# Performance work log

Measured on AMD Instinct MI355X. Metric: run time of the kernel, lower is better.

The kernel has to match this reference:

```python
import jax, jax.numpy as jnp
import numpy as np

NEG_SLOPE = 0.2


def setup_inputs() -> dict:
    key = jax.random.key(0)
    ks = jax.random.split(key, 6)
    N, E, IN, OUT = 100000, 1600000, 128, 64
    x = jax.random.normal(ks[0], (N, IN), dtype=jnp.float32)
    edge_index = jax.random.randint(ks[1], (2, E), 0, N, dtype=jnp.int64)
    W = jax.random.normal(ks[2], (IN, OUT), dtype=jnp.float32) * (1.0 / np.sqrt(IN))
    att_src = jax.random.normal(ks[3], (OUT,), dtype=jnp.float32) * (1.0 / np.sqrt(OUT))
    att_dst = jax.random.normal(ks[4], (OUT,), dtype=jnp.float32) * (1.0 / np.sqrt(OUT))
    bias = jnp.zeros((OUT,), dtype=jnp.float32)
    return {"x": x, "edge_index": edge_index, "W": W,
            "att_src": att_src, "att_dst": att_dst, "bias": bias}


def reference(x, edge_index, W, att_src, att_dst, bias):
    N = x.shape[0]
    # PyG GATConv default: add self loops
    loop = jnp.arange(N, dtype=edge_index.dtype)
    src = jnp.concatenate([edge_index[0], loop])  # message sources j
    dst = jnp.concatenate([edge_index[1], loop])  # message targets i

    h = x @ W                                      # [N, out]
    a_s = h @ att_src                              # [N]
    a_d = h @ att_dst                              # [N]

    # per-edge unnormalized attention logits (leaky relu, slope 0.2)
    e = jax.nn.leaky_relu(a_s[src] + a_d[dst], negative_slope=NEG_SLOPE)  # [E+N]

    # segment softmax over edges grouped by destination node
    seg_max = jax.ops.segment_max(e, dst, num_segments=N)  # [N]
    e_exp = jnp.exp(e - seg_max[dst])
    seg_sum = jax.ops.segment_sum(e_exp, dst, num_segments=N)  # [N], >0 via self loops
    alpha = e_exp / seg_sum[dst]                                # [E+N]

    # weighted scatter-add aggregation
    out = jax.ops.segment_sum(alpha[:, None] * h[src], dst, num_segments=N)  # [N, out]
    return out + bias
```

## Files before the change

### kernel.cpp

```cpp
#include <hip/hip_runtime.h>
#include <hip/hip_bf16.h>
#include <math.h>

#define NEG_SLOPE 0.2f
#define BSH    7
#define BNODES 128
#define CAP    2560
#define MAXB   1024
#define NCHUNK 256
#define CEMAX  6272
#define SMEMB  39424

typedef __attribute__((ext_vector_type(8))) short bf16x8;
typedef __attribute__((ext_vector_type(4))) float f32x4;

__device__ __forceinline__ float leaky(float v) { return v >= 0.0f ? v : NEG_SLOPE * v; }
__device__ __forceinline__ int clampi(int v, int lo, int hi) {
    return v < lo ? lo : (v > hi ? hi : v);
}
__device__ __forceinline__ float bflo(unsigned u) { return __uint_as_float(u << 16); }
__device__ __forceinline__ float bfhi(unsigned u) { return __uint_as_float(u & 0xFFFF0000u); }
__device__ __forceinline__ unsigned short f2bf(float f) {
    unsigned u = __float_as_uint(f);
    return (unsigned short)((u + 0x7FFFu + ((u >> 16) & 1u)) >> 16);
}
__device__ __forceinline__ bf16x8 pack8(float4 a, float4 b) {
    bf16x8 r;
    r[0] = (short)f2bf(a.x); r[1] = (short)f2bf(a.y);
    r[2] = (short)f2bf(a.z); r[3] = (short)f2bf(a.w);
    r[4] = (short)f2bf(b.x); r[5] = (short)f2bf(b.y);
    r[6] = (short)f2bf(b.z); r[7] = (short)f2bf(b.w);
    return r;
}

__global__ __launch_bounds__(512) void k_fused(
    const float* __restrict__ x, const float* __restrict__ W,
    const float* __restrict__ att_src, const float* __restrict__ att_dst,
    __hip_bfloat16* __restrict__ h, float* __restrict__ a_s,
    float* __restrict__ a_d, const int* __restrict__ ei,
    unsigned* __restrict__ binned, int* __restrict__ offc,
    int N, int E, int CE, int nb_lin)
{
    __shared__ int4 smem4[SMEMB / 16];
    const int tid = threadIdx.x;

    if ((int)blockIdx.x < nb_lin) {
        short* wlds = (short*)smem4;

        for (int idx = tid; idx < 1024; idx += 512) {
            int f = idx >> 6, L = idx & 63;
            int t = f >> 2, k0i = f & 3;
            int kbase = k0i * 32 + (L >> 4) * 8;
            int c = t * 16 + (L & 15);
            unsigned short v[8];
#pragma unroll
            for (int j = 0; j < 8; ++j) v[j] = f2bf(W[(kbase + j) * 64 + c]);
            uint4 p;
            p.x = (unsigned)v[0] | ((unsigned)v[1] << 16);
            p.y = (unsigned)v[2] | ((unsigned)v[3] << 16);
            p.z = (unsigned)v[4] | ((unsigned)v[5] << 16);
            p.w = (unsigned)v[6] | ((unsigned)v[7] << 16);
            ((uint4*)wlds)[idx] = p;
        }
        __syncthreads();

        const int lane = tid & 63;
        const int w    = tid >> 6;
        const int base = blockIdx.x * 128 + w * 16;
        const int m    = lane & 15;
        const int quad = lane >> 4;

        int rowc = min(base + m, N - 1);
        const float4* xr = (const float4*)x + (size_t)rowc * 32;

        bf16x8 afrag[4];
#pragma unroll
        for (int k0i = 0; k0i < 4; ++k0i) {
            float4 f0 = xr[k0i * 8 + quad * 2 + 0];
            float4 f1 = xr[k0i * 8 + quad * 2 + 1];
            afrag[k0i] = pack8(f0, f1);
        }

        f32x4 acc[4];
#pragma unroll
        for (int t = 0; t < 4; ++t) acc[t] = (f32x4){0.f, 0.f, 0.f, 0.f};

        const bf16x8* wf = (const bf16x8*)wlds;
#pragma unroll
        for (int t = 0; t < 4; ++t) {
#pragma unroll
            for (int k0i = 0; k0i < 4; ++k0i) {
                bf16x8 bfr = wf[(t * 4 + k0i) * 64 + lane];
                acc[t] = __builtin_amdgcn_mfma_f32_16x16x32_bf16(afrag[k0i], bfr, acc[t], 0, 0, 0);
            }
        }

        float ps[4] = {0.f, 0.f, 0.f, 0.f};
        float pd[4] = {0.f, 0.f, 0.f, 0.f};
#pragma unroll
        for (int t = 0; t < 4; ++t) {
            float as_c = att_src[t * 16 + m];
            float ad_c = att_dst[t * 16 + m];
#pragma unroll
            for (int q = 0; q < 4; ++q) {
                ps[q] = fmaf(acc[t][q], as_c, ps[q]);
                pd[q] = fmaf(acc[t][q], ad_c, pd[q]);
            }
        }
#pragma unroll
        for (int t = 0; t < 4; ++t) {
#pragma unroll
            for (int q = 0; q < 4; ++q) {
                int n = base + quad * 4 + q;
                if (n < N) h[(size_t)n * 64 + t * 16 + m] = __float2bfloat16(acc[t][q]);
            }
        }
#pragma unroll
        for (int q = 0; q < 4; ++q) {
            ps[q] += __shfl_xor(ps[q], 1, 64);
            ps[q] += __shfl_xor(ps[q], 2, 64);
            ps[q] += __shfl_xor(ps[q], 4, 64);
            ps[q] += __shfl_xor(ps[q], 8, 64);
            pd[q] += __shfl_xor(pd[q], 1, 64);
            pd[q] += __shfl_xor(pd[q], 2, 64);
            pd[q] += __shfl_xor(pd[q], 4, 64);
            pd[q] += __shfl_xor(pd[q], 8, 64);
        }
        if (m == 0) {
#pragma unroll
            for (int q = 0; q < 4; ++q) {
                int n = base + quad * 4 + q;
                if (n < N) { a_s[n] = ps[q]; a_d[n] = pd[q]; }
            }
        }
    } else {
        int* hist = (int*)smem4;
        int* off  = hist + MAXB;
        int* cur  = off + MAXB;
        int* s    = cur + MAXB;
        unsigned* stage = (unsigned*)(s + 512);

        const int c  = (int)blockIdx.x - nb_lin;
        const int e0 = c * CE;
        const int e1 = min(E, e0 + CE);
        const int ne = e1 - e0;

        for (int i = tid; i < MAXB; i += 512) hist[i] = 0;
        __syncthreads();
        for (int e = e0 + tid; e < e1; e += 512) {
            int dst = clampi(ei[E + e], 0, N - 1);
            atomicAdd(&hist[dst >> BSH], 1);
        }
        __syncthreads();
        int a0 = hist[2 * tid], a1 = hist[2 * tid + 1];
        int psum = a0 + a1;
        s[tid] = psum;
        __syncthreads();
        for (int d = 1; d < 512; d <<= 1) {
            int v = (tid >= d) ? s[tid - d] : 0;
            __syncthreads();
            s[tid] += v;
            __syncthreads();
        }
        int excl = s[tid] - psum;
        off[2 * tid]     = excl;
        off[2 * tid + 1] = excl + a0;
        cur[2 * tid]     = excl;
        cur[2 * tid + 1] = excl + a0;
        __syncthreads();
        for (int e = e0 + tid; e < e1; e += 512) {
            int src = clampi(ei[e],     0, N - 1);
            int dst = clampi(ei[E + e], 0, N - 1);
            int pos = atomicAdd(&cur[dst >> BSH], 1);
            stage[clampi(pos, 0, CEMAX - 1)] =
                ((unsigned)(dst & (BNODES - 1)) << 17) | (unsigned)src;
        }
        __syncthreads();
        for (int i = tid; i < ne; i += 512) binned[e0 + i] = stage[i];
        int* oc = offc + (size_t)c * (MAXB + 1);
        for (int i = tid; i < MAXB; i += 512) oc[i] = off[i];
        if (tid == 0) oc[MAXB] = ne;
    }
}

__global__ __launch_bounds__(512) void k_agg(
    const unsigned* __restrict__ binned, const int* __restrict__ offc,
    const float* __restrict__ a_s, const float* __restrict__ a_d,
    const __hip_bfloat16* __restrict__ hm, const float* __restrict__ bias,
    float* __restrict__ out, int N, int CE)
{
    __shared__ int   cnt[BNODES];
    __shared__ int   st[BNODES];
    __shared__ int   cur[BNODES];
    __shared__ float lsum[BNODES];
    __shared__ float wsl[BNODES];
    __shared__ float adl[BNODES];
    __shared__ int   runScan[NCHUNK + 1];
    __shared__ int   gbase[NCHUNK];
    __shared__ int   sc[NCHUNK];
    __shared__ unsigned eraw[CAP];
    __shared__ uint2 ew[CAP];

    const int tid   = threadIdx.x;
    const int b     = blockIdx.x;
    const int nbase = b << BSH;

    if (tid < BNODES) {
        cnt[tid] = 0;
        int n = nbase + tid;
        float as = 0.f, ad = 0.f;
        if (n < N) { as = a_s[n]; ad = a_d[n]; }
        adl[tid] = ad;
        float v = (n < N) ? __expf(leaky(as + ad)) : 0.f;
        wsl[tid]  = v;
        lsum[tid] = v;
    }
    int rc = 0;
    if (tid < NCHUNK) {
        const int* oc = offc + (size_t)tid * (MAXB + 1);
        int o0 = clampi(oc[b],     0, CE);
        int o1 = clampi(oc[b + 1], o0, CE);
        rc = o1 - o0;
        gbase[tid] = tid * CE + o0;
        sc[tid] = rc;
    }
    __syncthreads();
    for (int d = 1; d < NCHUNK; d <<= 1) {
        int v = (tid < NCHUNK && tid >= d) ? sc[tid - d] : 0;
        __syncthreads();
        if (tid < NCHUNK) sc[tid] += v;
        __syncthreads();
    }
    if (tid < NCHUNK) runScan[tid] = sc[tid] - rc;
    if (tid == NCHUNK - 1) runScan[NCHUNK] = sc[NCHUNK - 1];
    __syncthreads();
    int n_e = runScan[NCHUNK];
    if (n_e > CAP) n_e = CAP;

    for (int i = tid; i < n_e; i += 512) {
        int c = 0;
#pragma unroll
        for (int stp = NCHUNK >> 1; stp >= 1; stp >>= 1)
            if (runScan[c + stp] <= i) c += stp;
        eraw[i] = binned[(size_t)gbase[c] + (i - runScan[c])];
    }
    __syncthreads();
    for (int i = tid; i < n_e; i += 512)
        atomicAdd(&cnt[(eraw[i] >> 17) & (BNODES - 1)], 1);
    __syncthreads();
    if (tid < BNODES) st[tid] = cnt[tid];
    __syncthreads();
    for (int d = 1; d < BNODES; d <<= 1) {
        int v = (tid < BNODES && tid >= d) ? st[tid - d] : 0;
        __syncthreads();
        if (tid < BNODES) st[tid] += v;
        __syncthreads();
    }
    if (tid < BNODES) { st[tid] -= cnt[tid]; cur[tid] = st[tid]; }
    __syncthreads();
    for (int i = tid; i < n_e; i += 512) {
        unsigned pk = eraw[i];
        int ld  = (int)(pk >> 17) & (BNODES - 1);
        int src = (int)(pk & 0x1FFFFu);
        float wv = __expf(leaky(a_s[src] + adl[ld]));
        int pos = atomicAdd(&cur[ld], 1);
        if (pos < CAP) ew[pos] = make_uint2((unsigned)src, __float_as_uint(wv));
        atomicAdd(&lsum[ld], wv);
    }
    __syncthreads();

    const int lane = tid & 63;
    const int w    = tid >> 6;
    const int q    = lane & 7;
    const int p    = lane >> 3;
    const uint4*  h4 = (const uint4*)hm;
    const float4* b4 = (const float4*)bias;
    const float4 bb0 = b4[2 * q];
    const float4 bb1 = b4[2 * q + 1];

#pragma unroll 1
    for (int t = 0; t < 2; ++t) {
        int ln = t * 64 + w * 8 + p;
        int n  = nbase + ln;
        if (n >= N) continue;
        int deg = cnt[ln];
        int s0  = st[ln];
        if (s0 > CAP) s0 = CAP;
        if (deg > CAP - s0) deg = CAP - s0;

        float wself = wsl[ln];
        uint4 U = h4[(size_t)n * 8 + q];
        float acc0 = wself * bflo(U.x), acc1 = wself * bfhi(U.x);
        float acc2 = wself * bflo(U.y), acc3 = wself * bfhi(U.y);
        float acc4 = wself * bflo(U.z), acc5 = wself * bfhi(U.z);
        float acc6 = wself * bflo(U.w), acc7 = wself * bfhi(U.w);

        float wc = 0.f;
        if (deg > 0) {
            uint2 e0 = ew[s0];
            wc = __uint_as_float(e0.y);
            U  = h4[(size_t)e0.x * 8 + q];
        }
        for (int j = 0; j < deg; ++j) {
            uint4 U2 = make_uint4(0u, 0u, 0u, 0u);
            float w2 = 0.f;
            if (j + 1 < deg) {
                uint2 e1 = ew[s0 + j + 1];
                w2 = __uint_as_float(e1.y);
                U2 = h4[(size_t)e1.x * 8 + q];
            }
            acc0 = fmaf(wc, bflo(U.x), acc0);
            acc1 = fmaf(wc, bfhi(U.x), acc1);
            acc2 = fmaf(wc, bflo(U.y), acc2);
            acc3 = fmaf(wc, bfhi(U.y), acc3);
            acc4 = fmaf(wc, bflo(U.z), acc4);
            acc5 = fmaf(wc, bfhi(U.z), acc5);
            acc6 = fmaf(wc, bflo(U.w), acc6);
            acc7 = fmaf(wc, bfhi(U.w), acc7);
            U = U2; wc = w2;
        }

        float inv = 1.0f / lsum[ln];
        float4 o0, o1;
        o0.x = bb0.x + acc0 * inv;
        o0.y = bb0.y + acc1 * inv;
        o0.z = bb0.z + acc2 * inv;
        o0.w = bb0.w + acc3 * inv;
        o1.x = bb1.x + acc4 * inv;
        o1.y = bb1.y + acc5 * inv;
        o1.z = bb1.z + acc6 * inv;
        o1.w = bb1.w + acc7 * inv;
        float4* o4 = (float4*)out;
        o4[(size_t)n * 16 + 2 * q + 0] = o0;
        o4[(size_t)n * 16 + 2 * q + 1] = o1;
    }
}

extern "C" void kernel_launch(void* const* d_in, const int* in_sizes, int n_in,
                              void* d_out, int out_size, void* d_ws, size_t ws_size,
                              hipStream_t stream)
{
    const float* x       = (const float*)d_in[0];
    const int*   ei      = (const int*)d_in[1];
    const float* W       = (const float*)d_in[2];
    const float* att_src = (const float*)d_in[3];
    const float* att_dst = (const float*)d_in[4];
    const float* bias    = (const float*)d_in[5];
    float*       out     = (float*)d_out;

    const int N = in_sizes[0] / 128;
    const int E = in_sizes[1] / 2;

    __hip_bfloat16* h      = (__hip_bfloat16*)d_ws;
    float*          a_s    = (float*)(h + (size_t)N * 64);
    float*          a_d    = a_s + N;
    int*            offc   = (int*)(a_d + N);
    unsigned*       binned = (unsigned*)(offc + NCHUNK * (MAXB + 1));

    const int CE = (E + NCHUNK - 1) / NCHUNK;
    const int NB = (N + BNODES - 1) >> BSH;
    const int nb_lin = (N + 127) / 128;

    k_fused<<<nb_lin + NCHUNK, 512, 0, stream>>>(x, W, att_src, att_dst,
                                                 h, a_s, a_d, ei, binned, offc,
                                                 N, E, CE, nb_lin);
    k_agg  <<<NB,              512, 0, stream>>>(binned, offc, a_s, a_d, h,
                                                 bias, out, N, CE);
}
```

Baseline: 168.8 us.

## Deepen gather prefetch, sort nodes by degree, and swizzle blocks across XCDs

The aggregation loop now keeps four neighbor-row gathers in flight instead of one, so more memory latency is hidden per wave. Nodes in a block are bitonic-sorted by degree and paired high/low across two passes so the wave groups carry more even loads. Block indices are remapped per XCD so adjacent node ranges run on the same die's L2, and launch bounds now request higher occupancy. The cost is extra registers, extra barriers for the sort, and added tail-handling logic.

```diff
diff --git a/kernel.cpp b/kernel.cpp
--- a/kernel.cpp
+++ b/kernel.cpp
@@ -31,6 +31,13 @@
     r[4] = (short)f2bf(b.x); r[5] = (short)f2bf(b.y);
     r[6] = (short)f2bf(b.z); r[7] = (short)f2bf(b.w);
     return r;
+}
+__device__ __forceinline__ int xcd_swz(int orig, int nwg) {
+    int xcd = orig & 7;
+    int i   = orig >> 3;
+    int qq  = nwg >> 3, rr = nwg & 7;
+    int base = (xcd < rr) ? xcd * (qq + 1) : rr * (qq + 1) + (xcd - rr) * qq;
+    return base + i;
 }
 
 __global__ __launch_bounds__(512) void k_fused(
@@ -183,7 +190,19 @@
     }
 }
 
-__global__ __launch_bounds__(512) void k_agg(
+#define CONS(Uv, wv) \
+    acc0 = fmaf(wv, bflo(Uv.x), acc0); \
+    acc1 = fmaf(wv, bfhi(Uv.x), acc1); \
+    acc2 = fmaf(wv, bflo(Uv.y), acc2); \
+    acc3 = fmaf(wv, bfhi(Uv.y), acc3); \
+    acc4 = fmaf(wv, bflo(Uv.z), acc4); \
+    acc5 = fmaf(wv, bfhi(Uv.z), acc5); \
+    acc6 = fmaf(wv, bflo(Uv.w), acc6); \
+    acc7 = fmaf(wv, bfhi(Uv.w), acc7);
+#define LOADE(idx, Uv, wv) { uint2 _ee = ew[s0 + (idx)]; \
+    wv = __uint_as_float(_ee.y); Uv = h4[(size_t)_ee.x * 8 + q]; }
+
+__global__ __launch_bounds__(512, 8) void k_agg(
     const unsigned* __restrict__ binned, const int* __restrict__ offc,
     const float* __restrict__ a_s, const float* __restrict__ a_d,
     const __hip_bfloat16* __restrict__ hm, const float* __restrict__ bias,
@@ -195,6 +214,7 @@
     __shared__ float lsum[BNODES];
     __shared__ float wsl[BNODES];
     __shared__ float adl[BNODES];
+    __shared__ unsigned skey[BNODES];
     __shared__ int   runScan[NCHUNK + 1];
     __shared__ int   gbase[NCHUNK];
     __shared__ int   sc[NCHUNK];
@@ -202,7 +222,7 @@
     __shared__ uint2 ew[CAP];
 
     const int tid   = threadIdx.x;
-    const int b     = blockIdx.x;
+    const int b     = xcd_swz((int)blockIdx.x, (int)gridDim.x);
     const int nbase = b << BSH;
 
     if (tid < BNODES) {
@@ -267,6 +287,21 @@
         if (pos < CAP) ew[pos] = make_uint2((unsigned)src, __float_as_uint(wv));
         atomicAdd(&lsum[ld], wv);
     }
+    if (tid < BNODES) skey[tid] = ((unsigned)cnt[tid] << 7) | (unsigned)tid;
+    for (int k = 2; k <= BNODES; k <<= 1) {
+        for (int jj = k >> 1; jj > 0; jj >>= 1) {
+            __syncthreads();
+            if (tid < BNODES) {
+                int ixj = tid ^ jj;
+                if (ixj > tid) {
+                    unsigned va = skey[tid], vb = skey[ixj];
+                    if ((((tid & k) == 0)) == (va > vb)) {
+                        skey[tid] = vb; skey[ixj] = va;
+                    }
+                }
+            }
+        }
+    }
     __syncthreads();
 
     const int lane = tid & 63;
@@ -279,13 +314,14 @@
     const float4 bb1 = b4[2 * q + 1];
 
 #pragma unroll 1
-    for (int t = 0; t < 2; ++t) {
-        int ln = t * 64 + w * 8 + p;
-        int n  = nbase + ln;
+    for (int pass = 0; pass < 2; ++pass) {
+        int grp = (pass == 0) ? w : (15 - w);
+        int ln  = (int)(skey[grp * 8 + p] & 127u);
+        int n   = nbase + ln;
         if (n >= N) continue;
-        int deg = cnt[ln];
         int s0  = st[ln];
         if (s0 > CAP) s0 = CAP;
+        int deg = cnt[ln];
         if (deg > CAP - s0) deg = CAP - s0;
 
         float wself = wsl[ln];
@@ -295,29 +331,28 @@
         float acc4 = wself * bflo(U.z), acc5 = wself * bfhi(U.z);
         float acc6 = wself * bflo(U.w), acc7 = wself * bfhi(U.w);
 
-        float wc = 0.f;
-        if (deg > 0) {
-            uint2 e0 = ew[s0];
-            wc = __uint_as_float(e0.y);
-            U  = h4[(size_t)e0.x * 8 + q];
-        }
-        for (int j = 0; j < deg; ++j) {
-            uint4 U2 = make_uint4(0u, 0u, 0u, 0u);
-            float w2 = 0.f;
-            if (j + 1 < deg) {
-                uint2 e1 = ew[s0 + j + 1];
-                w2 = __uint_as_float(e1.y);
-                U2 = h4[(size_t)e1.x * 8 + q];
-            }
-            acc0 = fmaf(wc, bflo(U.x), acc0);
-            acc1 = fmaf(wc, bfhi(U.x), acc1);
-            acc2 = fmaf(wc, bflo(U.y), acc2);
-            acc3 = fmaf(wc, bfhi(U.y), acc3);
-            acc4 = fmaf(wc, bflo(U.z), acc4);
-            acc5 = fmaf(wc, bfhi(U.z), acc5);
-            acc6 = fmaf(wc, bflo(U.w), acc6);
-            acc7 = fmaf(wc, bfhi(U.w), acc7);
-            U = U2; wc = w2;
+        uint4 UA = make_uint4(0,0,0,0), UB = UA, UC = UA, UD = UA;
+        float wa = 0.f, wb = 0.f, wcv = 0.f, wd = 0.f;
+        if (deg > 0) LOADE(0, UA, wa);
+        if (deg > 1) LOADE(1, UB, wb);
+        if (deg > 2) LOADE(2, UC, wcv);
+        if (deg > 3) LOADE(3, UD, wd);
+        int j = 0;
+        for (; j + 7 < deg; j += 4) {
+            CONS(UA, wa); LOADE(j + 4, UA, wa);
+            CONS(UB, wb); LOADE(j + 5, UB, wb);
+            CONS(UC, wcv); LOADE(j + 6, UC, wcv);
+            CONS(UD, wd); LOADE(j + 7, UD, wd);
+        }
+        if (j     < deg) { CONS(UA, wa); }
+        if (j + 1 < deg) { CONS(UB, wb); }
+        if (j + 2 < deg) { CONS(UC, wcv); }
+        if (j + 3 < deg) { CONS(UD, wd); }
+        for (int t2 = j + 4; t2 < deg; ++t2) {
+            uint2 e2 = ew[s0 + t2];
+            float wv = __uint_as_float(e2.y);
+            uint4 U2 = h4[(size_t)e2.x * 8 + q];
+            CONS(U2, wv);
         }
 
         float inv = 1.0f / lsum[ln];
```

Result: slower. 183.1 us (+8.5%).

## Replace barrier-heavy LDS scans with wavefront shuffle scans and XCD-swizzle agg blocks

Applied to the files above, without the earlier changes.

Swaps the block-wide Hillis-Steele scans, each doubling step bracketed by __syncthreads, for single-wavefront scans using __shfl_up, with each lane holding several elements. This cuts roughly 40 barriers per block in the binning and aggregation kernels and shrinks shared memory. It also folds the per-node count atomics into the edge gather loop, removing one pass and one barrier. Aggregation block indices are remapped so that neighbouring bins run on the same XCD, aiming for better L2 locality, though only one wavefront does the scan work while the others wait.

```diff
diff --git a/kernel.cpp b/kernel.cpp
--- a/kernel.cpp
+++ b/kernel.cpp
@@ -9,7 +9,7 @@
 #define MAXB   1024
 #define NCHUNK 256
 #define CEMAX  6272
-#define SMEMB  39424
+#define SMEMB  37376
 
 typedef __attribute__((ext_vector_type(8))) short bf16x8;
 typedef __attribute__((ext_vector_type(4))) float f32x4;
@@ -31,6 +31,13 @@
     r[4] = (short)f2bf(b.x); r[5] = (short)f2bf(b.y);
     r[6] = (short)f2bf(b.z); r[7] = (short)f2bf(b.w);
     return r;
+}
+__device__ __forceinline__ int xcd_swz(int orig, int nwg) {
+    int xcd = orig & 7;
+    int i   = orig >> 3;
+    int qq  = nwg >> 3, rr = nwg & 7;
+    int base = (xcd < rr) ? xcd * (qq + 1) : rr * (qq + 1) + (xcd - rr) * qq;
+    return base + i;
 }
 
 __global__ __launch_bounds__(512) void k_fused(
@@ -137,8 +144,7 @@
         int* hist = (int*)smem4;
         int* off  = hist + MAXB;
         int* cur  = off + MAXB;
-        int* s    = cur + MAXB;
-        unsigned* stage = (unsigned*)(s + 512);
+        unsigned* stage = (unsigned*)(cur + MAXB);
 
         const int c  = (int)blockIdx.x - nb_lin;
         const int e0 = c * CE;
@@ -152,21 +158,24 @@
             atomicAdd(&hist[dst >> BSH], 1);
         }
         __syncthreads();
-        int a0 = hist[2 * tid], a1 = hist[2 * tid + 1];
-        int psum = a0 + a1;
-        s[tid] = psum;
-        __syncthreads();
-        for (int d = 1; d < 512; d <<= 1) {
-            int v = (tid >= d) ? s[tid - d] : 0;
-            __syncthreads();
-            s[tid] += v;
-            __syncthreads();
-        }
-        int excl = s[tid] - psum;
-        off[2 * tid]     = excl;
-        off[2 * tid + 1] = excl + a0;
-        cur[2 * tid]     = excl;
-        cur[2 * tid + 1] = excl + a0;
+        if (tid < 64) {
+            int v[16]; int tsum = 0;
+#pragma unroll
+            for (int k = 0; k < 16; ++k) { v[k] = hist[tid * 16 + k]; tsum += v[k]; }
+            int incl = tsum;
+#pragma unroll
+            for (int d = 1; d < 64; d <<= 1) {
+                int t = __shfl_up(incl, d, 64);
+                if (tid >= d) incl += t;
+            }
+            int run = incl - tsum;
+#pragma unroll
+            for (int k = 0; k < 16; ++k) {
+                off[tid * 16 + k] = run;
+                cur[tid * 16 + k] = run;
+                run += v[k];
+            }
+        }
         __syncthreads();
         for (int e = e0 + tid; e < e1; e += 512) {
             int src = clampi(ei[e],     0, N - 1);
@@ -197,12 +206,11 @@
     __shared__ float adl[BNODES];
     __shared__ int   runScan[NCHUNK + 1];
     __shared__ int   gbase[NCHUNK];
-    __shared__ int   sc[NCHUNK];
     __shared__ unsigned eraw[CAP];
     __shared__ uint2 ew[CAP];
 
     const int tid   = threadIdx.x;
-    const int b     = blockIdx.x;
+    const int b     = xcd_swz((int)blockIdx.x, (int)gridDim.x);
     const int nbase = b << BSH;
 
     if (tid < BNODES) {
@@ -215,24 +223,31 @@
         wsl[tid]  = v;
         lsum[tid] = v;
     }
-    int rc = 0;
     if (tid < NCHUNK) {
         const int* oc = offc + (size_t)tid * (MAXB + 1);
         int o0 = clampi(oc[b],     0, CE);
         int o1 = clampi(oc[b + 1], o0, CE);
-        rc = o1 - o0;
-        gbase[tid] = tid * CE + o0;
-        sc[tid] = rc;
-    }
-    __syncthreads();
-    for (int d = 1; d < NCHUNK; d <<= 1) {
-        int v = (tid < NCHUNK && tid >= d) ? sc[tid - d] : 0;
-        __syncthreads();
-        if (tid < NCHUNK) sc[tid] += v;
-        __syncthreads();
-    }
-    if (tid < NCHUNK) runScan[tid] = sc[tid] - rc;
-    if (tid == NCHUNK - 1) runScan[NCHUNK] = sc[NCHUNK - 1];
+        gbase[tid]   = tid * CE + o0;
+        runScan[tid] = o1 - o0;
+    }
+    __syncthreads();
+    if (tid < 64) {
+        int v0 = runScan[tid * 4 + 0], v1 = runScan[tid * 4 + 1];
+        int v2 = runScan[tid * 4 + 2], v3 = runScan[tid * 4 + 3];
+        int tsum = v0 + v1 + v2 + v3;
+        int incl = tsum;
+#pragma unroll
+        for (int d = 1; d < 64; d <<= 1) {
+            int t = __shfl_up(incl, d, 64);
+            if (tid >= d) incl += t;
+        }
+        int excl = incl - tsum;
+        runScan[tid * 4 + 0] = excl;
+        runScan[tid * 4 + 1] = excl + v0;
+        runScan[tid * 4 + 2] = excl + v0 + v1;
+        runScan[tid * 4 + 3] = excl + v0 + v1 + v2;
+        if (tid == 63) runScan[NCHUNK] = incl;
+    }
     __syncthreads();
     int n_e = runScan[NCHUNK];
     if (n_e > CAP) n_e = CAP;
@@ -242,21 +257,24 @@
 #pragma unroll
         for (int stp = NCHUNK >> 1; stp >= 1; stp >>= 1)
             if (runScan[c + stp] <= i) c += stp;
-        eraw[i] = binned[(size_t)gbase[c] + (i - runScan[c])];
-    }
-    __syncthreads();
-    for (int i = tid; i < n_e; i += 512)
-        atomicAdd(&cnt[(eraw[i] >> 17) & (BNODES - 1)], 1);
-    __syncthreads();
-    if (tid < BNODES) st[tid] = cnt[tid];
-    __syncthreads();
-    for (int d = 1; d < BNODES; d <<= 1) {
-        int v = (tid < BNODES && tid >= d) ? st[tid - d] : 0;
-        __syncthreads();
-        if (tid < BNODES) st[tid] += v;
-        __syncthreads();
-    }
-    if (tid < BNODES) { st[tid] -= cnt[tid]; cur[tid] = st[tid]; }
+        unsigned pk = binned[(size_t)gbase[c] + (i - runScan[c])];
+        eraw[i] = pk;
+        atomicAdd(&cnt[(pk >> 17) & (BNODES - 1)], 1);
+    }
+    __syncthreads();
+    if (tid < 64) {
+        int v0 = cnt[tid * 2], v1 = cnt[tid * 2 + 1];
+        int tsum = v0 + v1;
+        int incl = tsum;
+#pragma unroll
+        for (int d = 1; d < 64; d <<= 1) {
+            int t = __shfl_up(incl, d, 64);
+            if (tid >= d) incl += t;
+        }
+        int excl = incl - tsum;
+        st[tid * 2]      = excl;      cur[tid * 2]      = excl;
+        st[tid * 2 + 1]  = excl + v0; cur[tid * 2 + 1]  = excl + v0;
+    }
     __syncthreads();
     for (int i = tid; i < n_e; i += 512) {
         unsigned pk = eraw[i];
```

Result: faster. 162.9 us (median of 2 runs) (-3.5%).
